# Kernel optimization log

Measured on AMD Instinct MI355X. Metric: run time of the kernel, lower is better.

## Reference

```python
import jax, jax.numpy as jnp
import numpy as np

B, S, D = 8, 2048, 1024
H = 4
K = D // 2          # expand_k = 0.5 -> key dim 512
V = D               # expand_v = 1.0 -> value dim 1024
DK, DV = K // H, V // H   # 128, 256
LOW_RANK = 16
GATE_LOGIT_NORM = 16.0
EPS = 1e-5
MLP_H = 4 * D


def _layernorm(x, g, b):
    mu = jnp.mean(x, axis=-1, keepdims=True)
    var = jnp.mean(jnp.square(x - mu), axis=-1, keepdims=True)
    return (x - mu) * jax.lax.rsqrt(var + EPS) * g + b


def _rmsnorm(x, w):
    ms = jnp.mean(jnp.square(x), axis=-1, keepdims=True)
    return x * jax.lax.rsqrt(ms + EPS) * w


def _gla(xn, Wq, Wk, Wv, Wg, Wgk1, Wgk2, bgk, gnorm_w, Wo):
    # projections ([B,S,D] @ [D,*]); weights stored as [in, out]
    q = (xn @ Wq).reshape(B, S, H, DK) * (DK ** -0.5)
    k = (xn @ Wk).reshape(B, S, H, DK)
    v = (xn @ Wv).reshape(B, S, H, DV)
    gk = jax.nn.log_sigmoid(xn @ Wgk1 @ Wgk2 + bgk) / GATE_LOGIT_NORM
    gk = gk.reshape(B, S, H, DK)

    def step(state, inp):
        qt, kt, vt, gt = inp                     # [B,H,DK], [B,H,DK], [B,H,DV], [B,H,DK]
        state = jnp.exp(gt)[..., None] * state + kt[..., None] * vt[..., None, :]
        ot = jnp.einsum('bhk,bhkv->bhv', qt, state)
        return state, ot

    init = jnp.zeros((B, H, DK, DV), xn.dtype)
    xs = (q.transpose(1, 0, 2, 3), k.transpose(1, 0, 2, 3),
          v.transpose(1, 0, 2, 3), gk.transpose(1, 0, 2, 3))
    _, o = jax.lax.scan(step, init, xs)          # o: [S,B,H,DV]
    o = o.transpose(1, 0, 2, 3)                  # [B,S,H,DV]

    g = (xn @ Wg).reshape(B, S, H, DV)
    o = _rmsnorm(o, gnorm_w) * g * jax.nn.sigmoid(g)   # RMSNorm + swish output gate
    return o.reshape(B, S, V) @ Wo


def setup_inputs() -> dict:
    key = jax.random.key(0)
    ks = jax.random.split(key, 16)
    sd = 0.02
    return {
        'x': jax.random.normal(ks[0], (B, S, D), jnp.float32),
        'ln1_g': jnp.ones((D,), jnp.float32),
        'ln1_b': jnp.zeros((D,), jnp.float32),
        'Wq': jax.random.normal(ks[1], (D, K), jnp.float32) * sd,
        'Wk': jax.random.normal(ks[2], (D, K), jnp.float32) * sd,
        'Wv': jax.random.normal(ks[3], (D, V), jnp.float32) * sd,
        'Wg': jax.random.normal(ks[4], (D, V), jnp.float32) * sd,
        'Wgk1': jax.random.normal(ks[5], (D, LOW_RANK), jnp.float32) * sd,
        'Wgk2': jax.random.normal(ks[6], (LOW_RANK, K), jnp.float32) * sd,
        'bgk': jnp.zeros((K,), jnp.float32),
        'gnorm_w': jnp.ones((DV,), jnp.float32),
        'Wo': jax.random.normal(ks[7], (V, D), jnp.float32) * sd,
        'ln2_g': jnp.ones((D,), jnp.float32),
        'ln2_b': jnp.zeros((D,), jnp.float32),
        'W1': jax.random.normal(ks[8], (D, MLP_H), jnp.float32) * sd,
        'b1': jnp.zeros((MLP_H,), jnp.float32),
        'W2': jax.random.normal(ks[9], (MLP_H, D), jnp.float32) * sd,
        'b2': jnp.zeros((D,), jnp.float32),
    }


def reference(x, ln1_g, ln1_b, Wq, Wk, Wv, Wg, Wgk1, Wgk2, bgk, gnorm_w, Wo,
              ln2_g, ln2_b, W1, b1, W2, b2):
    # pre-norm GLA block, eval mode (dropout = identity)
    attn_out = _gla(_layernorm(x, ln1_g, ln1_b), Wq, Wk, Wv, Wg, Wgk1, Wgk2, bgk, gnorm_w, Wo)
    x = x + attn_out
    h = _layernorm(x, ln2_g, ln2_b)
    h = jax.nn.gelu(h @ W1 + b1, approximate=False) @ W2 + b2
    return x + h
```

## Files before the change

### kernel.cpp

```cpp
#include <hip/hip_runtime.h>
#include <stdint.h>


typedef unsigned short u16t;
typedef __attribute__((ext_vector_type(8))) short bf16x8;
typedef __attribute__((ext_vector_type(4))) float f32x4;
typedef __attribute__((ext_vector_type(4))) unsigned short u16x4;

__device__ __forceinline__ float bf2f(unsigned short u){ union{unsigned int i; float f;} v; v.i=((unsigned int)u)<<16; return v.f; }
__device__ __forceinline__ unsigned short f2bf(float f){ union{unsigned int i; float f;} v; v.f=f; unsigned int r=v.i+0x7FFFu+((v.i>>16)&1u); return (unsigned short)(r>>16); }
__device__ __forceinline__ f32x4 cvt4(u16x4 u){ f32x4 r; r[0]=bf2f(u[0]); r[1]=bf2f(u[1]); r[2]=bf2f(u[2]); r[3]=bf2f(u[3]); return r; }

__device__ __forceinline__ float gelu_f(float t){
  const float t3 = t*t*t;
  const float y = 2.3021183f*t + 0.10295465f*t3;
  const float e = __builtin_amdgcn_exp2f(y);
  return t - t*__builtin_amdgcn_rcpf(e + 1.f);
}

__device__ __forceinline__ void gload_lds16(const unsigned short* g, unsigned short* l)
{
  __builtin_amdgcn_global_load_lds(
      (const __attribute__((address_space(1))) unsigned int*)g,
      (__attribute__((address_space(3))) unsigned int*)l,
      16, 0, 0);
}

__global__ void k_transpose_multi(const float* __restrict__ Wq, const float* __restrict__ Wk,
                                  const float* __restrict__ Wv, const float* __restrict__ Wg,
                                  const float* __restrict__ Wo, const float* __restrict__ W1,
                                  const float* __restrict__ W2,
                                  unsigned short* __restrict__ WPT, unsigned short* __restrict__ WOT,
                                  unsigned short* __restrict__ W1T, unsigned short* __restrict__ W2T)
{
  __shared__ float tile[32][33];
  int bid = blockIdx.x;
  const float* src; unsigned short* dst; int Kin, N, nx;
  if      (bid < 512)  { src=Wq; dst=WPT;                          Kin=1024; N=512;  nx=16;  }
  else if (bid < 1024) { src=Wk; dst=WPT+(size_t)512*1024;         Kin=1024; N=512;  nx=16;  bid-=512;  }
  else if (bid < 2048) { src=Wv; dst=WPT+(size_t)1024*1024;        Kin=1024; N=1024; nx=32;  bid-=1024; }
  else if (bid < 3072) { src=Wg; dst=WPT+(size_t)2048*1024;        Kin=1024; N=1024; nx=32;  bid-=2048; }
  else if (bid < 4096) { src=Wo; dst=WOT;                          Kin=1024; N=1024; nx=32;  bid-=3072; }
  else if (bid < 8192) { src=W1; dst=W1T;                          Kin=1024; N=4096; nx=128; bid-=4096; }
  else                 { src=W2; dst=W2T;                          Kin=4096; N=1024; nx=32;  bid-=8192; }
  const int n0 = (bid % nx)*32, k0 = (bid / nx)*32;
  const int tx = threadIdx.x, ty = threadIdx.y;
  #pragma unroll
  for (int i = 0; i < 4; ++i)
    tile[ty + i*8][tx] = src[(size_t)(k0 + ty + i*8)*N + n0 + tx];
  __syncthreads();
  #pragma unroll
  for (int i = 0; i < 4; ++i)
    dst[(size_t)(n0 + ty + i*8)*Kin + k0 + tx] = f2bf(tile[tx][ty + i*8]);
}

__global__ void k_wgk(const float* __restrict__ Wgk1, const float* __restrict__ Wgk2, unsigned short* __restrict__ dstT)
{
  const int idx = blockIdx.x*256 + threadIdx.x;
  const int i = idx & 1023, j = idx >> 10;
  float s = 0.f;
  #pragma unroll
  for (int r = 0; r < 16; ++r) s += Wgk1[i*16 + r] * Wgk2[r*512 + j];
  dstT[(size_t)j*1024 + i] = f2bf(s);
}

__global__ void k_vtrans(const unsigned short* __restrict__ proj, const unsigned short* __restrict__ kt,
                         unsigned short* __restrict__ vtg, unsigned short* __restrict__ ktt)
{
  __shared__ unsigned short tile[32][33];
  const int tt = blockIdx.x, zz = blockIdx.y, bh = blockIdx.z;
  const int b = bh >> 2, h = bh & 3;
  const int tx = threadIdx.x, ty = threadIdx.y;
  if (zz < 8) {
    const int dvt = zz;
    #pragma unroll
    for (int i = 0; i < 4; ++i)
      tile[ty + i*8][tx] = proj[((size_t)b*2048 + tt*32 + ty + i*8)*3584 + 1024 + h*256 + dvt*32 + tx];
    __syncthreads();
    #pragma unroll
    for (int i = 0; i < 4; ++i)
      vtg[((size_t)bh*256 + dvt*32 + ty + i*8)*2048 + tt*32 + tx] = tile[tx][ty + i*8];
  } else {
    const int dkt = zz - 8;
    #pragma unroll
    for (int i = 0; i < 4; ++i)
      tile[ty + i*8][tx] = kt[((size_t)bh*2048 + tt*32 + ty + i*8)*128 + dkt*32 + tx];
    __syncthreads();
    #pragma unroll
    for (int i = 0; i < 4; ++i)
      ktt[((size_t)bh*128 + dkt*32 + ty + i*8)*2048 + tt*32 + tx] = tile[tx][ty + i*8];
  }
}

__global__ __launch_bounds__(256) void k_layernorm(const float* __restrict__ x, const float* __restrict__ g,
                                                   const float* __restrict__ b, unsigned short* __restrict__ out)
{
  const int row = blockIdx.x, tid = threadIdx.x;
  const float4 xv = *(const float4*)&x[(size_t)row*1024 + tid*4];
  float s  = xv.x + xv.y + xv.z + xv.w;
  float sq = xv.x*xv.x + xv.y*xv.y + xv.z*xv.z + xv.w*xv.w;
  #pragma unroll
  for (int o = 32; o > 0; o >>= 1) { s += __shfl_xor(s, o); sq += __shfl_xor(sq, o); }
  __shared__ float red[8];
  const int w = tid >> 6;
  if ((tid & 63) == 0) { red[w] = s; red[4 + w] = sq; }
  __syncthreads();
  s  = red[0] + red[1] + red[2] + red[3];
  sq = red[4] + red[5] + red[6] + red[7];
  const float mu = s * (1.f/1024.f);
  const float var = sq * (1.f/1024.f) - mu*mu;
  const float rs = rsqrtf(var + 1e-5f);
  float xe[4] = {xv.x, xv.y, xv.z, xv.w};
  u16x4 o4;
  #pragma unroll
  for (int i = 0; i < 4; ++i) {
    const int c = tid*4 + i;
    o4[i] = f2bf((xe[i] - mu) * rs * g[c] + b[c]);
  }
  *(u16x4*)&out[(size_t)row*1024 + tid*4] = o4;
}

template<int EPI>
__global__ __launch_bounds__(1024, 3)
void gemm256(const unsigned short* __restrict__ A, const unsigned short* __restrict__ Bt,
             int N, int K,
             float* outF, unsigned short* outH,
             const float* resid, const float* bias)
{
  __shared__ __align__(16) unsigned short lds[65536];
  const int tid = threadIdx.x;
  const int lane = tid & 63, w = tid >> 6;
  const int wr = w >> 2, wc = w & 3;
  const int l15 = lane & 15, lq = lane >> 4;

  const int nwg = gridDim.x * gridDim.y;
  const int bid = blockIdx.y * gridDim.x + blockIdx.x;
  const int q = nwg >> 3, r = nwg & 7;
  const int xcd = bid & 7, lid = bid >> 3;
  const int sw = (xcd < r ? xcd*(q+1) : r*(q+1) + (xcd - r)*q) + lid;
  const int row0 = (sw / gridDim.x) * 256;
  const int col0 = (sw % gridDim.x) * 256;

  const int rA_ = tid >> 3;
  const int cswz = 8 * ((tid & 7) ^ (rA_ & 7));
  const unsigned short* baseA[2];
  const unsigned short* baseB[2];
  #pragma unroll
  for (int h = 0; h < 2; ++h) {
    baseA[h] = A  + (size_t)(row0 + h*128 + rA_) * K + cswz;
    baseB[h] = Bt + (size_t)(col0 + h*128 + rA_) * K + cswz;
  }

  const int NT = K >> 6;

  f32x4 acc[4][4];
  #pragma unroll
  for (int m = 0; m < 4; ++m)
    #pragma unroll
    for (int n = 0; n < 4; ++n) { acc[m][n][0]=0.f; acc[m][n][1]=0.f; acc[m][n][2]=0.f; acc[m][n][3]=0.f; }

  const int carA = (wr >> 1) * 8192;
  const int carB = 16384 + (wc >> 1) * 8192;
  const int rowA = (wr & 1) * 64;
  const int rowB = (wc & 1) * 64;
  const int co = (l15 & 7) * 8;

  #define STAGE4(T)                                                            \
    {                                                                          \
      const int dbase = ((T) & 1) * 32768;                                     \
      const int ktt2 = (T) << 6;                                               \
      gload_lds16(baseA[0] + ktt2, (unsigned short*)&lds[dbase +         w*512]); \
      gload_lds16(baseA[1] + ktt2, (unsigned short*)&lds[dbase +  8192 + w*512]); \
      gload_lds16(baseB[0] + ktt2, (unsigned short*)&lds[dbase + 16384 + w*512]); \
      gload_lds16(baseB[1] + ktt2, (unsigned short*)&lds[dbase + 24576 + w*512]); \
    }

  #define MMAH(BUF, H)                                                         \
    {                                                                          \
      bf16x8 af[4], bfr[4];                                                    \
      _Pragma("unroll")                                                        \
      for (int mm = 0; mm < 4; ++mm)                                           \
        af[mm] = *(const bf16x8*)&lds[(BUF) + carA + (rowA + mm*16 + l15)*64   \
                                      + (((H)*32 + lq*8) ^ co)];               \
      _Pragma("unroll")                                                        \
      for (int nn = 0; nn < 4; ++nn)                                           \
        bfr[nn] = *(const bf16x8*)&lds[(BUF) + carB + (rowB + nn*16 + l15)*64  \
                                       + (((H)*32 + lq*8) ^ co)];              \
      asm volatile("s_waitcnt lgkmcnt(0)" ::: "memory");                       \
      __builtin_amdgcn_sched_barrier(0);                                       \
      if (H) { __builtin_amdgcn_s_barrier(); }   \
      __builtin_amdgcn_s_setprio(1);                                           \
      _Pragma("unroll")                                                        \
      for (int mm = 0; mm < 4; ++mm)                                           \
        _Pragma("unroll")                                                      \
        for (int nn = 0; nn < 4; ++nn)                                         \
          acc[mm][nn] = __builtin_amdgcn_mfma_f32_16x16x32_bf16(               \
              af[mm], bfr[nn], acc[mm][nn], 0, 0, 0);                          \
      __builtin_amdgcn_s_setprio(0);                                           \
    }

  STAGE4(0);
  for (int t = 0; t < NT; ++t) {
    const int buf = (t & 1) * 32768;
    if (t + 1 < NT) {
      STAGE4(t + 1);
      asm volatile("s_waitcnt vmcnt(4)" ::: "memory");
    } else {
      asm volatile("s_waitcnt vmcnt(0)" ::: "memory");
    }
    __builtin_amdgcn_sched_barrier(0);
    __builtin_amdgcn_s_barrier();
    MMAH(buf, 0);
    MMAH(buf, 1);
  }
  #undef STAGE4
  #undef MMAH

  #pragma unroll
  for (int mm = 0; mm < 4; ++mm)
    #pragma unroll
    for (int nn = 0; nn < 4; ++nn)
      #pragma unroll
      for (int ii = 0; ii < 4; ++ii) {
        const int rr = row0 + wr*64 + mm*16 + lq*4 + ii;
        const int cc = col0 + wc*64 + nn*16 + l15;
        const size_t idx = (size_t)rr * N + cc;
        const float v = acc[mm][nn][ii];
        if constexpr (EPI == 0) {
          outH[idx] = f2bf(v);
        } else if constexpr (EPI == 1) {
          outF[idx] = v + resid[idx];
        } else if constexpr (EPI == 2) {
          outH[idx] = f2bf(gelu_f(v + bias[cc]));
        } else {
          outF[idx] = v + bias[cc] + resid[idx];
        }
      }
}

__global__ __launch_bounds__(128) void k_scanprep(const unsigned short* __restrict__ proj, const float* __restrict__ bgk,
                                                  unsigned short* __restrict__ qt, unsigned short* __restrict__ kt,
                                                  float* __restrict__ eac)
{
  const int c = blockIdx.x & 31, bh = blockIdx.x >> 5;
  const int b = bh >> 2, h = bh & 3;
  const int dk = threadIdx.x;
  const size_t tok0 = (size_t)b*2048 + c*64;
  const float bg = bgk[h*128 + dk];
  float A = 0.f, ea = 1.f;
  for (int t = 0; t < 64; ++t) {
    const size_t prow = (tok0 + t) * 3584;
    const float qv = bf2f(proj[prow + h*128 + dk]);
    const float kv = bf2f(proj[prow + 512 + h*128 + dk]);
    const float z = bf2f(proj[prow + 3072 + h*128 + dk]) + bg;
    const float az = fabsf(z);
    const float sp = fmaxf(-z, 0.f)
                   + 0.69314718f*__builtin_amdgcn_logf(1.f + __builtin_amdgcn_exp2f(-1.44269504f*az));
    A -= sp * 0.0625f;
    ea = __builtin_amdgcn_exp2f(A * 1.44269504f);
    const float em = __builtin_amdgcn_rcpf(ea);
    const size_t orow = ((size_t)bh*2048 + c*64 + t)*128 + dk;
    qt[orow] = f2bf(qv * ea * 0.08838834764831845f);
    kt[orow] = f2bf(kv * em);
  }
  eac[((size_t)bh*32 + c)*128 + dk] = ea;
}

__global__ __launch_bounds__(512) void k_seqstate(const unsigned short* __restrict__ ktt,
                                                  const unsigned short* __restrict__ vtg,
                                                  const float* __restrict__ eac,
                                                  unsigned short* __restrict__ sst)
{
  __shared__ __align__(16) unsigned short SLq[16384];
  const int bid = blockIdx.x;
  const int bh = bid >> 3, dks = (bid >> 2) & 1, dvs = bid & 3;
  const int tid = threadIdx.x, lane = tid & 63, w = tid >> 6;
  const int wr = w >> 2, wc = w & 3;
  const int l15 = lane & 15, lq = lane >> 4;
  const int kc8 = (lane & 7) * 8;

  #define SSTAGE(C, BUF)                                                        \
    { { const int o = w*512 + lane*8;                                           \
        const int dkl = o >> 6;                                                 \
        gload_lds16(&ktt[((size_t)bh*128 + dks*64 + dkl)*2048 + (C)*64 + (kc8 ^ ((dkl & 7) << 3))], \
                    (unsigned short*)&SLq[(BUF)*8192 + w*512]); }                \
      { const int o = w*512 + lane*8;                                           \
        const int dvl = o >> 6;                                                 \
        gload_lds16(&vtg[((size_t)bh*256 + dvs*64 + dvl)*2048 + (C)*64 + (kc8 ^ ((dvl & 7) << 3))], \
                    (unsigned short*)&SLq[(BUF)*8192 + 4096 + w*512]); } }

  f32x4 acc[2];
  acc[0][0]=0.f; acc[0][1]=0.f; acc[0][2]=0.f; acc[0][3]=0.f;
  acc[1] = acc[0];

  SSTAGE(0, 0);
  asm volatile("s_waitcnt vmcnt(0)" ::: "memory");
  __builtin_amdgcn_sched_barrier(0);
  __builtin_amdgcn_s_barrier();

  for (int c = 0; c < 32; ++c) {
    const int buf = c & 1;
    if (c + 1 < 32) {
      SSTAGE(c + 1, buf ^ 1);
      asm volatile("s_waitcnt vmcnt(2)" ::: "memory");
    } else {
      asm volatile("s_waitcnt vmcnt(0)" ::: "memory");
    }
    __builtin_amdgcn_sched_barrier(0);
    __builtin_amdgcn_s_barrier();

    const size_t srow = (((size_t)bh*32 + c)*256 + dvs*64 + wc*16 + l15)*128;
    #pragma unroll
    for (int mm = 0; mm < 2; ++mm) {
      u16x4 tj;
      tj[0]=f2bf(acc[mm][0]); tj[1]=f2bf(acc[mm][1]); tj[2]=f2bf(acc[mm][2]); tj[3]=f2bf(acc[mm][3]);
      *(u16x4*)&sst[srow + dks*64 + wr*32 + mm*16 + lq*4] = tj;
    }
    f32x4 ev[2];
    #pragma unroll
    for (int mm = 0; mm < 2; ++mm)
      ev[mm] = *(const f32x4*)&eac[(size_t)(bh*32 + c)*128 + dks*64 + wr*32 + mm*16 + lq*4];

    const int base = buf*8192;
    bf16x8 afr[2][2], bfrg[2];
    #pragma unroll
    for (int mm = 0; mm < 2; ++mm) {
      const int rl = wr*32 + mm*16 + l15;
      const int co = (rl & 7) << 3;
      afr[mm][0] = *(const bf16x8*)&SLq[base + rl*64 + ((lq*8) ^ co)];
      afr[mm][1] = *(const bf16x8*)&SLq[base + rl*64 + ((32 + lq*8) ^ co)];
    }
    {
      const int dvl = wc*16 + l15;
      const int co = (dvl & 7) << 3;
      bfrg[0] = *(const bf16x8*)&SLq[base + 4096 + dvl*64 + ((lq*8) ^ co)];
      bfrg[1] = *(const bf16x8*)&SLq[base + 4096 + dvl*64 + ((32 + lq*8) ^ co)];
    }
    asm volatile("s_waitcnt lgkmcnt(0)" ::: "memory");
    __builtin_amdgcn_sched_barrier(0);
    #pragma unroll
    for (int k4 = 0; k4 < 2; ++k4)
      #pragma unroll
      for (int mm = 0; mm < 2; ++mm)
        acc[mm] = __builtin_amdgcn_mfma_f32_16x16x32_bf16(afr[mm][k4], bfrg[k4], acc[mm], 0, 0, 0);
    #pragma unroll
    for (int mm = 0; mm < 2; ++mm)
      #pragma unroll
      for (int i = 0; i < 4; ++i)
        acc[mm][i] *= ev[mm][i];
    __builtin_amdgcn_s_barrier();
  }
  #undef SSTAGE
}

__global__ __launch_bounds__(512) void k_attn_out(const unsigned short* __restrict__ qt,
                                                  const unsigned short* __restrict__ kt,
                                                  const unsigned short* __restrict__ vtg,
                                                  const unsigned short* __restrict__ sst,
                                                  const unsigned short* __restrict__ proj,
                                                  const float* __restrict__ gnw,
                                                  unsigned short* __restrict__ og)
{
  __shared__ __align__(16) unsigned short SL[61440];
  __shared__ float ssq[64];
  const int c = blockIdx.x & 31, bh = blockIdx.x >> 5;
  const int b = bh >> 2, h = bh & 3;
  const int tid = threadIdx.x, lane = tid & 63, w = tid >> 6;
  const int wr = w >> 2, wc = w & 3;
  const int l15 = lane & 15, lq = lane >> 4;
  const size_t qk0 = (size_t)bh*2048 + c*64;
  const size_t tok0 = (size_t)b*2048 + c*64;
  const int key15 = (l15 & 7) << 3;

  if (tid < 64) ssq[tid] = 0.f;

  const int kc8 = (lane & 7) * 8;
  #pragma unroll
  for (int it = 0; it < 2; ++it) {
    const int o = it*4096 + w*512 + lane*8;
    const int ch = o >> 12, r = (o >> 6) & 63;
    gload_lds16(&kt[(qk0 + r)*128 + ch*64 + (kc8 ^ ((r & 7) << 3))],
                (unsigned short*)&SL[53248 + it*4096 + w*512]);
  }
  #pragma unroll
  for (int it = 0; it < 4; ++it) {
    const int o = it*4096 + w*512 + lane*8;
    const int dv = o >> 6;
    gload_lds16(&vtg[((size_t)bh*256 + dv)*2048 + c*64 + (kc8 ^ ((dv & 7) << 3))],
                (unsigned short*)&SL[4096 + it*4096 + w*512]);
  }
  #pragma unroll
  for (int it = 0; it < 8; ++it) {
    const int o = it*4096 + w*512 + lane*8;
    const int ch = o >> 14, dv = (o >> 6) & 255;
    gload_lds16(&sst[((size_t)(bh*32 + c)*256 + dv)*128 + ch*64 + (kc8 ^ ((dv & 7) << 3))],
                (unsigned short*)&SL[20480 + it*4096 + w*512]);
  }
  bf16x8 aq[2][4];
  #pragma unroll
  for (int mm = 0; mm < 2; ++mm)
    #pragma unroll
    for (int k4 = 0; k4 < 4; ++k4)
      aq[mm][k4] = *(const bf16x8*)&qt[(qk0 + wr*32 + mm*16 + l15)*128 + k4*32 + lq*8];

  __syncthreads();

  f32x4 accp[2];
  accp[0][0]=0.f; accp[0][1]=0.f; accp[0][2]=0.f; accp[0][3]=0.f;
  accp[1] = accp[0];
  #pragma unroll
  for (int k4 = 0; k4 < 4; ++k4) {
    const int ch = k4 >> 1, k0c = (k4 & 1) * 32;
    const bf16x8 bk = *(const bf16x8*)&SL[53248 + ch*4096 + (wc*16 + l15)*64 + ((k0c + lq*8) ^ key15)];
    accp[0] = __builtin_amdgcn_mfma_f32_16x16x32_bf16(aq[0][k4], bk, accp[0], 0, 0, 0);
    accp[1] = __builtin_amdgcn_mfma_f32_16x16x32_bf16(aq[1][k4], bk, accp[1], 0, 0, 0);
  }
  #pragma unroll
  for (int mm = 0; mm < 2; ++mm)
    #pragma unroll
    for (int i = 0; i < 4; ++i) {
      const int rg = wr*32 + mm*16 + lq*4 + i;
      const int cg = wc*16 + l15;
      SL[rg*64 + (cg ^ ((rg & 7) << 3))] = f2bf((cg <= rg) ? accp[mm][i] : 0.f);
    }
  __syncthreads();

  f32x4 acco[2][4];
  #pragma unroll
  for (int mm = 0; mm < 2; ++mm)
    #pragma unroll
    for (int nn = 0; nn < 4; ++nn) { acco[mm][nn][0]=0.f; acco[mm][nn][1]=0.f; acco[mm][nn][2]=0.f; acco[mm][nn][3]=0.f; }

  #pragma unroll
  for (int t4 = 0; t4 < 2; ++t4) {
    bf16x8 ap[2];
    #pragma unroll
    for (int mm = 0; mm < 2; ++mm) {
      const int r = wr*32 + mm*16 + l15;
      ap[mm] = *(const bf16x8*)&SL[r*64 + ((t4*32 + lq*8) ^ key15)];
    }
    #pragma unroll
    for (int nn = 0; nn < 4; ++nn) {
      const int dv = wc*64 + nn*16 + l15;
      const bf16x8 bv = *(const bf16x8*)&SL[4096 + dv*64 + ((t4*32 + lq*8) ^ key15)];
      acco[0][nn] = __builtin_amdgcn_mfma_f32_16x16x32_bf16(ap[0], bv, acco[0][nn], 0, 0, 0);
      acco[1][nn] = __builtin_amdgcn_mfma_f32_16x16x32_bf16(ap[1], bv, acco[1][nn], 0, 0, 0);
    }
  }
  #pragma unroll
  for (int k4 = 0; k4 < 4; ++k4) {
    const int ch = k4 >> 1, k0c = (k4 & 1) * 32;
    #pragma unroll
    for (int nn = 0; nn < 4; ++nn) {
      const int dv = wc*64 + nn*16 + l15;
      const bf16x8 bs = *(const bf16x8*)&SL[20480 + ch*16384 + dv*64 + ((k0c + lq*8) ^ key15)];
      acco[0][nn] = __builtin_amdgcn_mfma_f32_16x16x32_bf16(aq[0][k4], bs, acco[0][nn], 0, 0, 0);
      acco[1][nn] = __builtin_amdgcn_mfma_f32_16x16x32_bf16(aq[1][k4], bs, acco[1][nn], 0, 0, 0);
    }
  }

  #pragma unroll
  for (int mm = 0; mm < 2; ++mm) {
    float part[4];
    #pragma unroll
    for (int i = 0; i < 4; ++i) {
      float s = 0.f;
      #pragma unroll
      for (int nn = 0; nn < 4; ++nn) s += acco[mm][nn][i]*acco[mm][nn][i];
      s += __shfl_xor(s, 1); s += __shfl_xor(s, 2); s += __shfl_xor(s, 4); s += __shfl_xor(s, 8);
      part[i] = s;
    }
    if (l15 == 0) {
      #pragma unroll
      for (int i = 0; i < 4; ++i)
        atomicAdd(&ssq[wr*32 + mm*16 + lq*4 + i], part[i]);
    }
  }
  __syncthreads();

  #pragma unroll
  for (int mm = 0; mm < 2; ++mm)
    #pragma unroll
    for (int i = 0; i < 4; ++i) {
      const int rg = wr*32 + mm*16 + lq*4 + i;
      const float rs = rsqrtf(ssq[rg] * (1.f/256.f) + 1e-5f);
      const size_t token = tok0 + rg;
      #pragma unroll
      for (int nn = 0; nn < 4; ++nn) {
        const int dv = wc*64 + nn*16 + l15;
        const float gf = bf2f(proj[token*3584 + 2048 + h*256 + dv]);
        const float swv = gf * __builtin_amdgcn_rcpf(1.f + __builtin_amdgcn_exp2f(-1.44269504f*gf));
        og[token*1024 + h*256 + dv] = f2bf(acco[mm][nn][i] * rs * gnw[dv] * swv);
      }
    }
}

extern "C" void kernel_launch(void* const* d_in, const int* in_sizes, int n_in,
                              void* d_out, int out_size, void* d_ws, size_t ws_size,
                              hipStream_t stream)
{
  (void)in_sizes; (void)n_in; (void)out_size; (void)ws_size;
  const float* x    = (const float*)d_in[0];
  const float* ln1g = (const float*)d_in[1];
  const float* ln1b = (const float*)d_in[2];
  const float* Wq   = (const float*)d_in[3];
  const float* Wk   = (const float*)d_in[4];
  const float* Wv   = (const float*)d_in[5];
  const float* Wg   = (const float*)d_in[6];
  const float* Wgk1 = (const float*)d_in[7];
  const float* Wgk2 = (const float*)d_in[8];
  const float* bgk  = (const float*)d_in[9];
  const float* gnw  = (const float*)d_in[10];
  const float* Wo   = (const float*)d_in[11];
  const float* ln2g = (const float*)d_in[12];
  const float* ln2b = (const float*)d_in[13];
  const float* W1   = (const float*)d_in[14];
  const float* b1   = (const float*)d_in[15];
  const float* W2   = (const float*)d_in[16];
  const float* b2   = (const float*)d_in[17];
  float* out = (float*)d_out;
  char* ws = (char*)d_ws;

  u16t*  XN   = (u16t*)(ws + 0);
  u16t*  KTT  = (u16t*)(ws + 0);
  u16t*  OG   = (u16t*)(ws + 0);
  u16t*  WPT  = (u16t*)(ws + 33554432);
  u16t*  WOT  = (u16t*)(ws + 40894464);
  u16t*  W1T  = (u16t*)(ws + 42991616);
  u16t*  W2T  = (u16t*)(ws + 51380224);
  u16t*  PROJ = (u16t*)(ws + 59768832);
  u16t*  QT   = (u16t*)(ws + 177209344);
  u16t*  KT   = (u16t*)(ws + 193986560);
  float* EAC  = (float*)(ws + 210763776);
  u16t*  VT   = (u16t*)(ws + 211288064);
  u16t*  H2   = (u16t*)(ws + 211288064);
  u16t*  HID  = PROJ;
  u16t*  SST  = (u16t*)d_out;

  k_transpose_multi<<<12288, dim3(32,8), 0, stream>>>(Wq, Wk, Wv, Wg, Wo, W1, W2, WPT, WOT, W1T, W2T);
  k_wgk<<<2048, 256, 0, stream>>>(Wgk1, Wgk2, WPT + (size_t)3072*1024);

  k_layernorm<<<16384, 256, 0, stream>>>(x, ln1g, ln1b, XN);
  gemm256<0><<<dim3(14,64), 1024, 0, stream>>>(XN, WPT, 3584, 1024, nullptr, PROJ, nullptr, nullptr);
  k_scanprep<<<1024, 128, 0, stream>>>(PROJ, bgk, QT, KT, EAC);
  k_vtrans<<<dim3(64,12,32), dim3(32,8), 0, stream>>>(PROJ, KT, VT, KTT);
  k_seqstate<<<256, 512, 0, stream>>>(KTT, VT, EAC, SST);
  k_attn_out<<<1024, 512, 0, stream>>>(QT, KT, VT, SST, PROJ, gnw, OG);
  gemm256<1><<<dim3(4,64),  1024, 0, stream>>>(OG, WOT, 1024, 1024, out, nullptr, x, nullptr);
  k_layernorm<<<16384, 256, 0, stream>>>(out, ln2g, ln2b, H2);
  gemm256<2><<<dim3(16,64), 1024, 0, stream>>>(H2, W1T, 4096, 1024, nullptr, HID, nullptr, b1);
  gemm256<3><<<dim3(4,64),  1024, 0, stream>>>(HID, W2T, 1024, 4096, out, nullptr, out, b2);
}
```

Before: 672.4 us.

## Shrink GEMM tiles to 128x256 with 512 threads and K-step of 32

The shared GEMM kernel moves from a 256x256 tile with 16 waves and 64-wide K slices to a 128x256 tile with 8 waves and 32-wide K slices. LDS use drops from 128KB to 48KB so more workgroups can share a CU, and the LDS swizzle pattern is rewritten for 32-element rows. All four GEMM launches double the grid rows. The aim is better occupancy and latency hiding, at the cost of less operand reuse per tile and twice as many barriers per unit of K.

```diff
diff --git a/kernel.cpp b/kernel.cpp
--- a/kernel.cpp
+++ b/kernel.cpp
@@ -121,13 +121,13 @@
 }
 
 template<int EPI>
-__global__ __launch_bounds__(1024, 3)
+__global__ __launch_bounds__(512, 4)
 void gemm256(const unsigned short* __restrict__ A, const unsigned short* __restrict__ Bt,
              int N, int K,
              float* outF, unsigned short* outH,
              const float* resid, const float* bias)
 {
-  __shared__ __align__(16) unsigned short lds[65536];
+  __shared__ __align__(16) unsigned short lds[24576];
   const int tid = threadIdx.x;
   const int lane = tid & 63, w = tid >> 6;
   const int wr = w >> 2, wc = w & 3;
@@ -138,20 +138,18 @@
   const int q = nwg >> 3, r = nwg & 7;
   const int xcd = bid & 7, lid = bid >> 3;
   const int sw = (xcd < r ? xcd*(q+1) : r*(q+1) + (xcd - r)*q) + lid;
-  const int row0 = (sw / gridDim.x) * 256;
+  const int row0 = (sw / gridDim.x) * 128;
   const int col0 = (sw % gridDim.x) * 256;
 
-  const int rA_ = tid >> 3;
-  const int cswz = 8 * ((tid & 7) ^ (rA_ & 7));
-  const unsigned short* baseA[2];
+  const int rowS = tid >> 2;
+  const int csw  = ((tid & 3) ^ ((rowS >> 1) & 3)) * 8;
+  const unsigned short* baseA    = A  + (size_t)(row0 + rowS) * K + csw;
   const unsigned short* baseB[2];
   #pragma unroll
-  for (int h = 0; h < 2; ++h) {
-    baseA[h] = A  + (size_t)(row0 + h*128 + rA_) * K + cswz;
-    baseB[h] = Bt + (size_t)(col0 + h*128 + rA_) * K + cswz;
-  }
-
-  const int NT = K >> 6;
+  for (int L = 0; L < 2; ++L)
+    baseB[L] = Bt + (size_t)(col0 + L*128 + rowS) * K + csw;
+
+  const int NT = K >> 5;
 
   f32x4 acc[4][4];
   #pragma unroll
@@ -159,62 +157,52 @@
     #pragma unroll
     for (int n = 0; n < 4; ++n) { acc[m][n][0]=0.f; acc[m][n][1]=0.f; acc[m][n][2]=0.f; acc[m][n][3]=0.f; }
 
-  const int carA = (wr >> 1) * 8192;
-  const int carB = 16384 + (wc >> 1) * 8192;
-  const int rowA = (wr & 1) * 64;
-  const int rowB = (wc & 1) * 64;
-  const int co = (l15 & 7) * 8;
-
-  #define STAGE4(T)                                                            \
+  const int rk = (l15 >> 1) & 3;
+
+  #define STAGE3(T)                                                            \
     {                                                                          \
-      const int dbase = ((T) & 1) * 32768;                                     \
-      const int ktt2 = (T) << 6;                                               \
-      gload_lds16(baseA[0] + ktt2, (unsigned short*)&lds[dbase +         w*512]); \
-      gload_lds16(baseA[1] + ktt2, (unsigned short*)&lds[dbase +  8192 + w*512]); \
-      gload_lds16(baseB[0] + ktt2, (unsigned short*)&lds[dbase + 16384 + w*512]); \
-      gload_lds16(baseB[1] + ktt2, (unsigned short*)&lds[dbase + 24576 + w*512]); \
-    }
-
-  #define MMAH(BUF, H)                                                         \
-    {                                                                          \
-      bf16x8 af[4], bfr[4];                                                    \
-      _Pragma("unroll")                                                        \
-      for (int mm = 0; mm < 4; ++mm)                                           \
-        af[mm] = *(const bf16x8*)&lds[(BUF) + carA + (rowA + mm*16 + l15)*64   \
-                                      + (((H)*32 + lq*8) ^ co)];               \
-      _Pragma("unroll")                                                        \
-      for (int nn = 0; nn < 4; ++nn)                                           \
-        bfr[nn] = *(const bf16x8*)&lds[(BUF) + carB + (rowB + nn*16 + l15)*64  \
-                                       + (((H)*32 + lq*8) ^ co)];              \
-      asm volatile("s_waitcnt lgkmcnt(0)" ::: "memory");                       \
-      __builtin_amdgcn_sched_barrier(0);                                       \
-      if (H) { __builtin_amdgcn_s_barrier(); }   \
-      __builtin_amdgcn_s_setprio(1);                                           \
-      _Pragma("unroll")                                                        \
-      for (int mm = 0; mm < 4; ++mm)                                           \
-        _Pragma("unroll")                                                      \
-        for (int nn = 0; nn < 4; ++nn)                                         \
-          acc[mm][nn] = __builtin_amdgcn_mfma_f32_16x16x32_bf16(               \
-              af[mm], bfr[nn], acc[mm][nn], 0, 0, 0);                          \
-      __builtin_amdgcn_s_setprio(0);                                           \
-    }
-
-  STAGE4(0);
+      const int dbase = ((T) & 1) * 12288;                                     \
+      const int kt2 = (T) << 5;                                                \
+      gload_lds16(baseA    + kt2, (unsigned short*)&lds[dbase +        w*512]); \
+      gload_lds16(baseB[0] + kt2, (unsigned short*)&lds[dbase + 4096 + w*512]); \
+      gload_lds16(baseB[1] + kt2, (unsigned short*)&lds[dbase + 8192 + w*512]); \
+    }
+
+  STAGE3(0);
   for (int t = 0; t < NT; ++t) {
-    const int buf = (t & 1) * 32768;
+    const int dbase = (t & 1) * 12288;
     if (t + 1 < NT) {
-      STAGE4(t + 1);
-      asm volatile("s_waitcnt vmcnt(4)" ::: "memory");
+      STAGE3(t + 1);
+      asm volatile("s_waitcnt vmcnt(3)" ::: "memory");
     } else {
       asm volatile("s_waitcnt vmcnt(0)" ::: "memory");
     }
     __builtin_amdgcn_sched_barrier(0);
     __builtin_amdgcn_s_barrier();
-    MMAH(buf, 0);
-    MMAH(buf, 1);
-  }
-  #undef STAGE4
-  #undef MMAH
+
+    bf16x8 af[4], bfr[4];
+    #pragma unroll
+    for (int mm = 0; mm < 4; ++mm) {
+      const int rA = wr*64 + mm*16 + l15;
+      af[mm] = *(const bf16x8*)&lds[dbase + rA*32 + ((lq ^ rk) * 8)];
+    }
+    #pragma unroll
+    for (int nn = 0; nn < 4; ++nn) {
+      const int rB = wc*64 + nn*16 + l15;
+      bfr[nn] = *(const bf16x8*)&lds[dbase + 4096 + rB*32 + ((lq ^ rk) * 8)];
+    }
+    asm volatile("s_waitcnt lgkmcnt(0)" ::: "memory");
+    __builtin_amdgcn_sched_barrier(0);
+    __builtin_amdgcn_s_setprio(1);
+    #pragma unroll
+    for (int mm = 0; mm < 4; ++mm)
+      #pragma unroll
+      for (int nn = 0; nn < 4; ++nn)
+        acc[mm][nn] = __builtin_amdgcn_mfma_f32_16x16x32_bf16(af[mm], bfr[nn], acc[mm][nn], 0, 0, 0);
+    __builtin_amdgcn_s_setprio(0);
+    __builtin_amdgcn_s_barrier();
+  }
+  #undef STAGE3
 
   #pragma unroll
   for (int mm = 0; mm < 4; ++mm)
@@ -541,13 +529,13 @@
   k_wgk<<<2048, 256, 0, stream>>>(Wgk1, Wgk2, WPT + (size_t)3072*1024);
 
   k_layernorm<<<16384, 256, 0, stream>>>(x, ln1g, ln1b, XN);
-  gemm256<0><<<dim3(14,64), 1024, 0, stream>>>(XN, WPT, 3584, 1024, nullptr, PROJ, nullptr, nullptr);
+  gemm256<0><<<dim3(14,128), 512, 0, stream>>>(XN, WPT, 3584, 1024, nullptr, PROJ, nullptr, nullptr);
   k_scanprep<<<1024, 128, 0, stream>>>(PROJ, bgk, QT, KT, EAC);
   k_vtrans<<<dim3(64,12,32), dim3(32,8), 0, stream>>>(PROJ, KT, VT, KTT);
   k_seqstate<<<256, 512, 0, stream>>>(KTT, VT, EAC, SST);
   k_attn_out<<<1024, 512, 0, stream>>>(QT, KT, VT, SST, PROJ, gnw, OG);
-  gemm256<1><<<dim3(4,64),  1024, 0, stream>>>(OG, WOT, 1024, 1024, out, nullptr, x, nullptr);
+  gemm256<1><<<dim3(4,128),  512, 0, stream>>>(OG, WOT, 1024, 1024, out, nullptr, x, nullptr);
   k_layernorm<<<16384, 256, 0, stream>>>(out, ln2g, ln2b, H2);
-  gemm256<2><<<dim3(16,64), 1024, 0, stream>>>(H2, W1T, 4096, 1024, nullptr, HID, nullptr, b1);
-  gemm256<3><<<dim3(4,64),  1024, 0, stream>>>(HID, W2T, 1024, 4096, out, nullptr, out, b2);
-}
+  gemm256<2><<<dim3(16,128), 512, 0, stream>>>(H2, W1T, 4096, 1024, nullptr, HID, nullptr, b1);
+  gemm256<3><<<dim3(4,128),  512, 0, stream>>>(HID, W2T, 1024, 4096, out, nullptr, out, b2);
+}
```

Measured after the change: 713.1 us. 1.06x slower.

## Compute low-rank gate via rank-16 factors instead of folding into projection GEMM

Applied to the files above, without the earlier changes.

Stops pre-multiplying Wgk1·Wgk2 into a dense 1024x512 weight appended to the fused projection GEMM. A new small kernel computes XN·Wgk1 (rank 16) per token, and scanprep expands it with Wgk2 in registers. This shrinks the main projection GEMM from 3584 to 3072 output columns and removes the wgk precompute kernel. In exchange it adds an extra pass over XN, scalar FMA work in scanprep, and a temporary buffer that aliases the output.

```diff
diff --git a/kernel.cpp b/kernel.cpp
--- a/kernel.cpp
+++ b/kernel.cpp
@@ -54,14 +54,32 @@
     dst[(size_t)(n0 + ty + i*8)*Kin + k0 + tx] = f2bf(tile[tx][ty + i*8]);
 }
 
-__global__ void k_wgk(const float* __restrict__ Wgk1, const float* __restrict__ Wgk2, unsigned short* __restrict__ dstT)
-{
-  const int idx = blockIdx.x*256 + threadIdx.x;
-  const int i = idx & 1023, j = idx >> 10;
-  float s = 0.f;
-  #pragma unroll
-  for (int r = 0; r < 16; ++r) s += Wgk1[i*16 + r] * Wgk2[r*512 + j];
-  dstT[(size_t)j*1024 + i] = f2bf(s);
+__global__ __launch_bounds__(256) void k_zgemm(const unsigned short* __restrict__ XN,
+                                               const float* __restrict__ Wgk1,
+                                               float* __restrict__ zg)
+{
+  __shared__ float Wg1s[128*16];
+  __shared__ unsigned short XNs[16*136];
+  const int token0 = blockIdx.x * 16;
+  const int tid = threadIdx.x;
+  const int tt = tid >> 4, j = tid & 15;
+  float acc = 0.f;
+  for (int cb = 0; cb < 8; ++cb) {
+    __syncthreads();
+    #pragma unroll
+    for (int i = 0; i < 8; ++i)
+      Wg1s[i*256 + tid] = Wgk1[(size_t)cb*2048 + i*256 + tid];
+    {
+      const int r = tid >> 4, cc = (tid & 15) * 8;
+      *(u16x4*)&XNs[r*136 + cc]     = *(const u16x4*)&XN[(size_t)(token0 + r)*1024 + cb*128 + cc];
+      *(u16x4*)&XNs[r*136 + cc + 4] = *(const u16x4*)&XN[(size_t)(token0 + r)*1024 + cb*128 + cc + 4];
+    }
+    __syncthreads();
+    #pragma unroll 4
+    for (int c = 0; c < 128; ++c)
+      acc += bf2f(XNs[tt*136 + c]) * Wg1s[c*16 + j];
+  }
+  zg[(size_t)(token0 + tt)*16 + j] = acc;
 }
 
 __global__ void k_vtrans(const unsigned short* __restrict__ proj, const unsigned short* __restrict__ kt,
@@ -75,7 +93,7 @@
     const int dvt = zz;
     #pragma unroll
     for (int i = 0; i < 4; ++i)
-      tile[ty + i*8][tx] = proj[((size_t)b*2048 + tt*32 + ty + i*8)*3584 + 1024 + h*256 + dvt*32 + tx];
+      tile[ty + i*8][tx] = proj[((size_t)b*2048 + tt*32 + ty + i*8)*3072 + 1024 + h*256 + dvt*32 + tx];
     __syncthreads();
     #pragma unroll
     for (int i = 0; i < 4; ++i)
@@ -238,21 +256,37 @@
       }
 }
 
-__global__ __launch_bounds__(128) void k_scanprep(const unsigned short* __restrict__ proj, const float* __restrict__ bgk,
+__global__ __launch_bounds__(128) void k_scanprep(const unsigned short* __restrict__ proj,
+                                                  const float* __restrict__ zg,
+                                                  const float* __restrict__ Wgk2,
+                                                  const float* __restrict__ bgk,
                                                   unsigned short* __restrict__ qt, unsigned short* __restrict__ kt,
                                                   float* __restrict__ eac)
 {
+  __shared__ float ZGs[1024];
   const int c = blockIdx.x & 31, bh = blockIdx.x >> 5;
   const int b = bh >> 2, h = bh & 3;
   const int dk = threadIdx.x;
   const size_t tok0 = (size_t)b*2048 + c*64;
-  const float bg = bgk[h*128 + dk];
+  #pragma unroll
+  for (int it = 0; it < 8; ++it)
+    ZGs[it*128 + dk] = zg[tok0*16 + it*128 + dk];
+  __syncthreads();
+
+  const int col = h*128 + dk;
+  const float bg = bgk[col];
+  float w2[16];
+  #pragma unroll
+  for (int r2 = 0; r2 < 16; ++r2) w2[r2] = Wgk2[r2*512 + col];
+
   float A = 0.f, ea = 1.f;
   for (int t = 0; t < 64; ++t) {
-    const size_t prow = (tok0 + t) * 3584;
+    const size_t prow = (tok0 + t) * 3072;
     const float qv = bf2f(proj[prow + h*128 + dk]);
     const float kv = bf2f(proj[prow + 512 + h*128 + dk]);
-    const float z = bf2f(proj[prow + 3072 + h*128 + dk]) + bg;
+    float z = bg;
+    #pragma unroll
+    for (int r2 = 0; r2 < 16; ++r2) z += ZGs[t*16 + r2] * w2[r2];
     const float az = fabsf(z);
     const float sp = fmaxf(-z, 0.f)
                    + 0.69314718f*__builtin_amdgcn_logf(1.f + __builtin_amdgcn_exp2f(-1.44269504f*az));
@@ -326,15 +360,15 @@
     #pragma unroll
     for (int mm = 0; mm < 2; ++mm) {
       const int rl = wr*32 + mm*16 + l15;
-      const int co = (rl & 7) << 3;
-      afr[mm][0] = *(const bf16x8*)&SLq[base + rl*64 + ((lq*8) ^ co)];
-      afr[mm][1] = *(const bf16x8*)&SLq[base + rl*64 + ((32 + lq*8) ^ co)];
+      const int co2 = (rl & 7) << 3;
+      afr[mm][0] = *(const bf16x8*)&SLq[base + rl*64 + ((lq*8) ^ co2)];
+      afr[mm][1] = *(const bf16x8*)&SLq[base + rl*64 + ((32 + lq*8) ^ co2)];
     }
     {
       const int dvl = wc*16 + l15;
-      const int co = (dvl & 7) << 3;
-      bfrg[0] = *(const bf16x8*)&SLq[base + 4096 + dvl*64 + ((lq*8) ^ co)];
-      bfrg[1] = *(const bf16x8*)&SLq[base + 4096 + dvl*64 + ((32 + lq*8) ^ co)];
+      const int co2 = (dvl & 7) << 3;
+      bfrg[0] = *(const bf16x8*)&SLq[base + 4096 + dvl*64 + ((lq*8) ^ co2)];
+      bfrg[1] = *(const bf16x8*)&SLq[base + 4096 + dvl*64 + ((32 + lq*8) ^ co2)];
     }
     asm volatile("s_waitcnt lgkmcnt(0)" ::: "memory");
     __builtin_amdgcn_sched_barrier(0);
@@ -488,7 +522,7 @@
       #pragma unroll
       for (int nn = 0; nn < 4; ++nn) {
         const int dv = wc*64 + nn*16 + l15;
-        const float gf = bf2f(proj[token*3584 + 2048 + h*256 + dv]);
+        const float gf = bf2f(proj[token*3072 + 2048 + h*256 + dv]);
         const float swv = gf * __builtin_amdgcn_rcpf(1.f + __builtin_amdgcn_exp2f(-1.44269504f*gf));
         og[token*1024 + h*256 + dv] = f2bf(acco[mm][nn][i] * rs * gnw[dv] * swv);
       }
@@ -536,13 +570,14 @@
   u16t*  H2   = (u16t*)(ws + 211288064);
   u16t*  HID  = PROJ;
   u16t*  SST  = (u16t*)d_out;
+  float* ZG   = (float*)d_out;
 
   k_transpose_multi<<<12288, dim3(32,8), 0, stream>>>(Wq, Wk, Wv, Wg, Wo, W1, W2, WPT, WOT, W1T, W2T);
-  k_wgk<<<2048, 256, 0, stream>>>(Wgk1, Wgk2, WPT + (size_t)3072*1024);
 
   k_layernorm<<<16384, 256, 0, stream>>>(x, ln1g, ln1b, XN);
-  gemm256<0><<<dim3(14,64), 1024, 0, stream>>>(XN, WPT, 3584, 1024, nullptr, PROJ, nullptr, nullptr);
-  k_scanprep<<<1024, 128, 0, stream>>>(PROJ, bgk, QT, KT, EAC);
+  k_zgemm<<<1024, 256, 0, stream>>>(XN, Wgk1, ZG);
+  gemm256<0><<<dim3(12,64), 1024, 0, stream>>>(XN, WPT, 3072, 1024, nullptr, PROJ, nullptr, nullptr);
+  k_scanprep<<<1024, 128, 0, stream>>>(PROJ, ZG, Wgk2, bgk, QT, KT, EAC);
   k_vtrans<<<dim3(64,12,32), dim3(32,8), 0, stream>>>(PROJ, KT, VT, KTT);
   k_seqstate<<<256, 512, 0, stream>>>(KTT, VT, EAC, SST);
   k_attn_out<<<1024, 512, 0, stream>>>(QT, KT, VT, SST, PROJ, gnw, OG);
```

After: 676.2 us. Within noise of the previous version (+0.6%).
